# Kernel tuning notes

Hardware: AMD Instinct MI355X
Metric: run time of the kernel (lower is better)

## Reference

```python
import jax, jax.numpy as jnp
import numpy as np

N_ATOMS = 131072
N_TYPES = 256
D_IN = 64
D_OUT = 64


def setup_inputs() -> dict:
    key = jax.random.key(0)
    k_x, k_t, k_w, k_b = jax.random.split(key, 4)
    x = jax.random.normal(k_x, (N_ATOMS, D_IN), dtype=jnp.float32)
    atom_types = jax.random.randint(k_t, (N_ATOMS,), 0, N_TYPES, dtype=jnp.int64)
    # Per-atom-type linear weights/biases (the 'unique' table gathered per atom).
    W = jax.random.normal(k_w, (N_TYPES, D_OUT, D_IN), dtype=jnp.float32) * (1.0 / np.sqrt(D_IN))
    b = jax.random.normal(k_b, (N_TYPES, D_OUT), dtype=jnp.float32) * 0.01
    return {"x": x, "atom_types": atom_types, "W": W, "b": b}


def reference(x, atom_types, W, b):
    # Gather type-specific linear params per atom (gather_unique_first semantics),
    # apply the per-atom linear, then tanh.
    Wg = W[atom_types]          # [N, d_out, d_in]
    bg = b[atom_types]          # [N, d_out]
    y = jnp.einsum('noi,ni->no', Wg, x) + bg  # [N, d_out]
    return jnp.tanh(y)
```

## Files before the change

kernel.cpp:

```cpp
#include <hip/hip_runtime.h>

#define N_ATOMS 131072
#define N_TYPES 256
#define D 64
#define CAP 1024
#define BPT 4

using sfrag = __attribute__((ext_vector_type(8))) short;
using ffrag = __attribute__((ext_vector_type(4))) float;

__device__ __forceinline__ short f2bf(float f)
{
    union { float f; unsigned u; } v; v.f = f;
    unsigned r = v.u + 0x7FFFu + ((v.u >> 16) & 1u);
    return (short)(r >> 16);
}

__device__ __forceinline__ float fast_tanh(float v)
{
    float e = __expf(2.0f * v);
    return 1.0f - __fdividef(2.0f, e + 1.0f);
}

__global__ __launch_bounds__(256) void scatter_kernel(
    const int* __restrict__ types, int* __restrict__ cursor, int* __restrict__ bucket)
{
    __shared__ int lhist[N_TYPES];
    __shared__ int lbase[N_TYPES];
    __shared__ int lcur[N_TYPES];
    const int tid  = threadIdx.x;
    const int base = blockIdx.x * 1024;
    lhist[tid] = 0;
    __syncthreads();

    int ty[4];
#pragma unroll
    for (int k = 0; k < 4; ++k) ty[k] = types[base + k * 256 + tid];
#pragma unroll
    for (int k = 0; k < 4; ++k) atomicAdd(&lhist[ty[k]], 1);
    __syncthreads();

    const int cnt = lhist[tid];
    if (cnt > 0) lbase[tid] = atomicAdd(&cursor[tid], cnt);
    lcur[tid] = 0;
    __syncthreads();

#pragma unroll
    for (int k = 0; k < 4; ++k) {
        const int t = ty[k];
        const int p = atomicAdd(&lcur[t], 1);
        const int q = lbase[t] + p;
        if (q < CAP) bucket[t * CAP + q] = base + k * 256 + tid;
    }
}

__global__ __launch_bounds__(256, 4) void apply_kernel(
    const float* __restrict__ x, const float* __restrict__ W,
    const float* __restrict__ b, const int* __restrict__ bucket,
    const int* __restrict__ cursor, float* __restrict__ out)
{
    const int t = blockIdx.x & 255;
    const int j = blockIdx.x >> 8;
    int n = cursor[t];
    if (n > CAP) n = CAP;

    const int wave = threadIdx.x >> 6;
    const int lane = threadIdx.x & 63;
    const int c = lane & 15;
    const int q = lane >> 4;

    const int*   bk = bucket + (size_t)t * CAP;
    const float* Wt = W + (size_t)t * (D * D);

    const int stride = BPT * 4;
    int g = j * 4 + wave;
    if (g * 16 >= n) return;

    int aidx;
    {
        int ridx = g * 16 + c;
        if (ridx >= n) ridx = n - 1;
        aidx = bk[ridx];
    }

    sfrag Bf[4][2];
#pragma unroll
    for (int nt = 0; nt < 4; ++nt) {
#pragma unroll
        for (int ks = 0; ks < 2; ++ks) {
            const float4* wr = (const float4*)(Wt + (size_t)(nt * 16 + c) * D + ks * 32 + q * 8);
            float4 w0 = wr[0], w1 = wr[1];
            sfrag f;
            f[0] = f2bf(w0.x); f[1] = f2bf(w0.y); f[2] = f2bf(w0.z); f[3] = f2bf(w0.w);
            f[4] = f2bf(w1.x); f[5] = f2bf(w1.y); f[6] = f2bf(w1.z); f[7] = f2bf(w1.w);
            Bf[nt][ks] = f;
        }
    }
    float bias[4];
#pragma unroll
    for (int nt = 0; nt < 4; ++nt) bias[nt] = b[(size_t)t * D + nt * 16 + c];

    float4 x0, x1, x2, x3;
    {
        const float4* xr = (const float4*)x + (size_t)aidx * 16 + q * 2;
        x0 = xr[0]; x1 = xr[1]; x2 = xr[8]; x3 = xr[9];
    }

    while (true) {
        const int gn = g + stride;
        const bool more = (gn * 16 < n);

        int naidx = 0; float4 nx0, nx1, nx2, nx3;
        if (more) {
            int ridx = gn * 16 + c;
            if (ridx >= n) ridx = n - 1;
            naidx = bk[ridx];
            const float4* xr = (const float4*)x + (size_t)naidx * 16 + q * 2;
            nx0 = xr[0]; nx1 = xr[1]; nx2 = xr[8]; nx3 = xr[9];
        }

        sfrag A0, A1;
        A0[0] = f2bf(x0.x); A0[1] = f2bf(x0.y); A0[2] = f2bf(x0.z); A0[3] = f2bf(x0.w);
        A0[4] = f2bf(x1.x); A0[5] = f2bf(x1.y); A0[6] = f2bf(x1.z); A0[7] = f2bf(x1.w);
        A1[0] = f2bf(x2.x); A1[1] = f2bf(x2.y); A1[2] = f2bf(x2.z); A1[3] = f2bf(x2.w);
        A1[4] = f2bf(x3.x); A1[5] = f2bf(x3.y); A1[6] = f2bf(x3.z); A1[7] = f2bf(x3.w);

        const int base = g * 16;
        int  oat[4]; bool ov[4];
#pragma unroll
        for (int r = 0; r < 4; ++r) {
            ov[r]  = (base + q * 4 + r) < n;
            oat[r] = __shfl(aidx, q * 4 + r, 64);
        }

#pragma unroll
        for (int nt = 0; nt < 4; ++nt) {
            ffrag acc = {0.f, 0.f, 0.f, 0.f};
            acc = __builtin_amdgcn_mfma_f32_16x16x32_bf16(A0, Bf[nt][0], acc, 0, 0, 0);
            acc = __builtin_amdgcn_mfma_f32_16x16x32_bf16(A1, Bf[nt][1], acc, 0, 0, 0);
#pragma unroll
            for (int r = 0; r < 4; ++r) {
                if (ov[r])
                    out[(size_t)oat[r] * D + nt * 16 + c] = fast_tanh(acc[r] + bias[nt]);
            }
        }

        if (!more) break;
        g = gn; aidx = naidx;
        x0 = nx0; x1 = nx1; x2 = nx2; x3 = nx3;
    }
}

extern "C" void kernel_launch(void* const* d_in, const int* in_sizes, int n_in,
                              void* d_out, int out_size, void* d_ws, size_t ws_size,
                              hipStream_t stream)
{
    const float* x     = (const float*)d_in[0];
    const int*   types = (const int*)  d_in[1];
    const float* W     = (const float*)d_in[2];
    const float* b     = (const float*)d_in[3];
    float*       out   = (float*)d_out;

    int* cursor = (int*)d_ws;
    int* bucket = (int*)((char*)d_ws + 1024);

    hipMemsetAsync(cursor, 0, N_TYPES * sizeof(int), stream);
    scatter_kernel<<<dim3(N_ATOMS / 1024), dim3(256), 0, stream>>>(types, cursor, bucket);
    apply_kernel<<<dim3(BPT * N_TYPES), dim3(256), 0, stream>>>(x, W, b, bucket, cursor, out);
}
```

Before: 107.1 us.

## Replace global atomics with per-block histogram prefix, prefetch two atom groups before cursor

```diff
diff --git a/kernel.cpp b/kernel.cpp
--- a/kernel.cpp
+++ b/kernel.cpp
@@ -5,6 +5,8 @@
 #define D 64
 #define CAP 1024
 #define BPT 4
+#define G_BLK (N_ATOMS / 1024)
+#define IDX_MASK (N_ATOMS - 1)
 
 using sfrag = __attribute__((ext_vector_type(8))) short;
 using ffrag = __attribute__((ext_vector_type(4))) float;
@@ -22,12 +24,10 @@
     return 1.0f - __fdividef(2.0f, e + 1.0f);
 }
 
-__global__ __launch_bounds__(256) void scatter_kernel(
-    const int* __restrict__ types, int* __restrict__ cursor, int* __restrict__ bucket)
+__global__ __launch_bounds__(256) void hist_kernel(
+    const int* __restrict__ types, int* __restrict__ bhist)
 {
     __shared__ int lhist[N_TYPES];
-    __shared__ int lbase[N_TYPES];
-    __shared__ int lcur[N_TYPES];
     const int tid  = threadIdx.x;
     const int base = blockIdx.x * 1024;
     lhist[tid] = 0;
@@ -40,11 +40,30 @@
     for (int k = 0; k < 4; ++k) atomicAdd(&lhist[ty[k]], 1);
     __syncthreads();
 
-    const int cnt = lhist[tid];
-    if (cnt > 0) lbase[tid] = atomicAdd(&cursor[tid], cnt);
-    lcur[tid] = 0;
+    bhist[blockIdx.x * N_TYPES + tid] = lhist[tid];
+}
+
+__global__ __launch_bounds__(256) void scatter_kernel(
+    const int* __restrict__ types, const int* __restrict__ bhist,
+    int* __restrict__ cursor, int* __restrict__ bucket)
+{
+    __shared__ int lbase[N_TYPES];
+    __shared__ int lcur[N_TYPES];
+    const int tid  = threadIdx.x;
+    const int blk  = blockIdx.x;
+    const int base = blk * 1024;
+
+    int s = 0;
+#pragma unroll 8
+    for (int b = 0; b < blk; ++b) s += bhist[b * N_TYPES + tid];
+    lbase[tid] = s;
+    lcur[tid]  = 0;
+    if (blk == G_BLK - 1) cursor[tid] = s + bhist[(G_BLK - 1) * N_TYPES + tid];
     __syncthreads();
 
+    int ty[4];
+#pragma unroll
+    for (int k = 0; k < 4; ++k) ty[k] = types[base + k * 256 + tid];
 #pragma unroll
     for (int k = 0; k < 4; ++k) {
         const int t = ty[k];
@@ -61,9 +80,6 @@
 {
     const int t = blockIdx.x & 255;
     const int j = blockIdx.x >> 8;
-    int n = cursor[t];
-    if (n > CAP) n = CAP;
-
     const int wave = threadIdx.x >> 6;
     const int lane = threadIdx.x & 63;
     const int c = lane & 15;
@@ -72,16 +88,16 @@
     const int*   bk = bucket + (size_t)t * CAP;
     const float* Wt = W + (size_t)t * (D * D);
 
-    const int stride = BPT * 4;
-    int g = j * 4 + wave;
-    if (g * 16 >= n) return;
+    const int g0 = j * 4 + wave;
+    const int g1 = g0 + 16;
 
-    int aidx;
-    {
-        int ridx = g * 16 + c;
-        if (ridx >= n) ridx = n - 1;
-        aidx = bk[ridx];
-    }
+    int i0 = bk[g0 * 16 + c] & IDX_MASK;
+    int i1 = bk[g1 * 16 + c] & IDX_MASK;
+
+    const float4* xr0 = (const float4*)x + (size_t)i0 * 16 + q * 2;
+    float4 a00 = xr0[0], a01 = xr0[1], a02 = xr0[8], a03 = xr0[9];
+    const float4* xr1 = (const float4*)x + (size_t)i1 * 16 + q * 2;
+    float4 a10 = xr1[0], a11 = xr1[1], a12 = xr1[8], a13 = xr1[9];
 
     sfrag Bf[4][2];
 #pragma unroll
@@ -100,39 +116,23 @@
 #pragma unroll
     for (int nt = 0; nt < 4; ++nt) bias[nt] = b[(size_t)t * D + nt * 16 + c];
 
-    float4 x0, x1, x2, x3;
-    {
-        const float4* xr = (const float4*)x + (size_t)aidx * 16 + q * 2;
-        x0 = xr[0]; x1 = xr[1]; x2 = xr[8]; x3 = xr[9];
-    }
+    int n = cursor[t];
+    if (n > CAP) n = CAP;
 
-    while (true) {
-        const int gn = g + stride;
-        const bool more = (gn * 16 < n);
-
-        int naidx = 0; float4 nx0, nx1, nx2, nx3;
-        if (more) {
-            int ridx = gn * 16 + c;
-            if (ridx >= n) ridx = n - 1;
-            naidx = bk[ridx];
-            const float4* xr = (const float4*)x + (size_t)naidx * 16 + q * 2;
-            nx0 = xr[0]; nx1 = xr[1]; nx2 = xr[8]; nx3 = xr[9];
-        }
-
+    auto compute = [&](int g, int aidx, float4 x0, float4 x1, float4 x2, float4 x3) {
         sfrag A0, A1;
         A0[0] = f2bf(x0.x); A0[1] = f2bf(x0.y); A0[2] = f2bf(x0.z); A0[3] = f2bf(x0.w);
         A0[4] = f2bf(x1.x); A0[5] = f2bf(x1.y); A0[6] = f2bf(x1.z); A0[7] = f2bf(x1.w);
         A1[0] = f2bf(x2.x); A1[1] = f2bf(x2.y); A1[2] = f2bf(x2.z); A1[3] = f2bf(x2.w);
         A1[4] = f2bf(x3.x); A1[5] = f2bf(x3.y); A1[6] = f2bf(x3.z); A1[7] = f2bf(x3.w);
 
-        const int base = g * 16;
+        const int gb = g * 16;
         int  oat[4]; bool ov[4];
 #pragma unroll
         for (int r = 0; r < 4; ++r) {
-            ov[r]  = (base + q * 4 + r) < n;
+            ov[r]  = (gb + q * 4 + r) < n;
             oat[r] = __shfl(aidx, q * 4 + r, 64);
         }
-
 #pragma unroll
         for (int nt = 0; nt < 4; ++nt) {
             ffrag acc = {0.f, 0.f, 0.f, 0.f};
@@ -144,10 +144,16 @@
                     out[(size_t)oat[r] * D + nt * 16 + c] = fast_tanh(acc[r] + bias[nt]);
             }
         }
+    };
 
-        if (!more) break;
-        g = gn; aidx = naidx;
-        x0 = nx0; x1 = nx1; x2 = nx2; x3 = nx3;
+    if (g0 * 16 < n) compute(g0, i0, a00, a01, a02, a03);
+    if (g1 * 16 < n) compute(g1, i1, a10, a11, a12, a13);
+
+    for (int g = g0 + 32; g * 16 < n; g += 16) {
+        int ii = bk[g * 16 + c] & IDX_MASK;
+        const float4* xr = (const float4*)x + (size_t)ii * 16 + q * 2;
+        float4 b0 = xr[0], b1 = xr[1], b2 = xr[8], b3 = xr[9];
+        compute(g, ii, b0, b1, b2, b3);
     }
 }
 
@@ -163,8 +169,9 @@
 
     int* cursor = (int*)d_ws;
     int* bucket = (int*)((char*)d_ws + 1024);
+    int* bhist  = (int*)((char*)d_ws + 1024 + (size_t)N_TYPES * CAP * sizeof(int));
 
-    hipMemsetAsync(cursor, 0, N_TYPES * sizeof(int), stream);
-    scatter_kernel<<<dim3(N_ATOMS / 1024), dim3(256), 0, stream>>>(types, cursor, bucket);
-    apply_kernel<<<dim3(BPT * N_TYPES), dim3(256), 0, stream>>>(x, W, b, bucket, cursor, out);
+    hist_kernel   <<<dim3(G_BLK), dim3(256), 0, stream>>>(types, bhist);
+    scatter_kernel<<<dim3(G_BLK), dim3(256), 0, stream>>>(types, bhist, cursor, bucket);
+    apply_kernel  <<<dim3(BPT * N_TYPES), dim3(256), 0, stream>>>(x, W, b, bucket, cursor, out);
 }
```

Measured after the change: 108.3 us. Within noise of the previous version (+1.0%).
